# Optimization experiments

Measured on AMD Instinct MI355X. Metric: run time of the kernel, lower is better.

The kernel has to match this reference:

```python
import jax, jax.numpy as jnp
import numpy as np

N_HEAD = 4

def _conv1x1(x, W, b):
    # x: (N, C, W, H), W: (Cout, Cin), b: (Cout,) -- 1x1 conv == channel matmul
    return jnp.einsum('nchw,oc->nohw', x, W) + b[None, :, None, None]

def setup_inputs() -> dict:
    key = jax.random.key(0)
    ks = jax.random.split(key, 8)
    B, T, Tq, C, R = 16, 128, 64, 64, 16
    s = 0.05
    return {
        'qq': jax.random.normal(ks[0], (B * Tq, C, R, R), dtype=jnp.float32),
        'kv': jax.random.normal(ks[1], (B, T, C, R, R), dtype=jnp.float32),
        'Wq': jax.random.normal(ks[2], (C, C), dtype=jnp.float32) * s,
        'bq': jnp.zeros((C,), dtype=jnp.float32),
        'Wk': jax.random.normal(ks[3], (C, C), dtype=jnp.float32) * s,
        'bk': jnp.zeros((C,), dtype=jnp.float32),
        'Wv': jax.random.normal(ks[4], (C, C), dtype=jnp.float32) * s,
        'bv': jnp.zeros((C,), dtype=jnp.float32),
    }

def reference(qq, kv, Wq, bq, Wk, bk, Wv, bv):
    B, T, C, W, H = kv.shape
    dh = C // N_HEAD
    kvf = kv.reshape(-1, C, W, H)  # (B*T, C, W, H)
    # project and split heads: (B, n, S, dh, W, H)
    q = _conv1x1(qq, Wq, bq).reshape(B, -1, N_HEAD, dh, W, H).transpose(0, 2, 1, 3, 4, 5)
    k = _conv1x1(kvf, Wk, bk).reshape(B, -1, N_HEAD, dh, W, H).transpose(0, 2, 1, 3, 4, 5)
    v = _conv1x1(kvf, Wv, bv).reshape(B, -1, N_HEAD, dh, W, H).transpose(0, 2, 1, 3, 4, 5)
    scale = 1.0 / np.sqrt(W * H * dh).astype(np.float32)
    sim = jnp.einsum('bnkcwh,bntcwh->bnkt', q, k) * scale
    sim = jax.nn.softmax(sim, axis=-1)
    out = jnp.einsum('bnkt,bntcwh->bnkcwh', sim, v)
    out = out.transpose(0, 2, 1, 3, 4, 5).reshape(qq.shape)
    return out, sim
```

## Files before the change

kernel.cpp:

```cpp
#include <hip/hip_runtime.h>
#include <hip/hip_bf16.h>
#include <stdint.h>
#include <stddef.h>

#define DEVI __device__ __forceinline__

typedef __attribute__((ext_vector_type(8)))  short bf16x8;
typedef __attribute__((ext_vector_type(4)))  float f32x4;
typedef __attribute__((ext_vector_type(16))) float f32x16;
typedef __attribute__((ext_vector_type(2)))  unsigned u32x2;

DEVI unsigned short f2bf(float f) {
    __hip_bfloat16 h = __float2bfloat16(f);
    union { __hip_bfloat16 h; unsigned short u; } v; v.h = h; return v.u;
}
DEVI unsigned pk2(float lo, float hi) {
    return (unsigned)f2bf(lo) | ((unsigned)f2bf(hi) << 16);
}
DEVI f32x4 zero4() { f32x4 z; z[0] = z[1] = z[2] = z[3] = 0.f; return z; }
DEVI f32x16 zero16() {
    f32x16 z;
#pragma unroll
    for (int i = 0; i < 16; ++i) z[i] = 0.f;
    return z;
}


DEVI void load_wfrags(const float* __restrict__ W, const float* __restrict__ B,
                      int l15, int lg, bf16x8 (&bf)[4][2], float (&bias)[4]) {
#pragma unroll
    for (int ot = 0; ot < 4; ++ot) {
        const int o = ot * 16 + l15;
        bias[ot] = B[o];
#pragma unroll
        for (int ks = 0; ks < 2; ++ks) {
            const float* wp = W + o * 64 + ks * 32 + lg * 8;
            f32x4 w0 = *(const f32x4*)wp, w1 = *(const f32x4*)(wp + 4);
            bf16x8 a;
#pragma unroll
            for (int j = 0; j < 4; ++j) { a[j] = (short)f2bf(w0[j]); a[4 + j] = (short)f2bf(w1[j]); }
            bf[ot][ks] = a;
        }
    }
}

DEVI void proj_emit(unsigned short* __restrict__ S, const bf16x8 (&afr)[4][2],
                    const bf16x8 (&bf)[4][2], const float (&bias)[4],
                    int tid, int w, int l15, int lg,
                    unsigned short* __restrict__ og) {
#pragma unroll
    for (int pt = 0; pt < 4; ++pt) {
        const int p = w * 64 + pt * 16 + lg * 4;
#pragma unroll
        for (int ot = 0; ot < 4; ++ot) {
            const int o = ot * 16 + l15;
            f32x4 a1 = zero4();
            a1 = __builtin_amdgcn_mfma_f32_16x16x32_bf16(afr[pt][0], bf[ot][0], a1, 0, 0, 0);
            a1 = __builtin_amdgcn_mfma_f32_16x16x32_bf16(afr[pt][1], bf[ot][1], a1, 0, 0, 0);
            u32x2 sv;
            sv[0] = pk2(a1[0] + bias[ot], a1[1] + bias[ot]);
            sv[1] = pk2(a1[2] + bias[ot], a1[3] + bias[ot]);
            *(u32x2*)(&S[o * 264 + p]) = sv;
        }
    }
    __syncthreads();
#pragma unroll
    for (int it = 0; it < 8; ++it) {
        const int idx = it * 256 + tid;
        const int o = idx >> 5, px = (idx & 31) * 8;
        f32x4 vv = *(const f32x4*)(&S[o * 264 + px]);
        *(f32x4*)(og + (size_t)o * 256 + px) = vv;
    }
}

__global__ __launch_bounds__(256) void proj_q_kernel(
    const float* __restrict__ qq, const float* __restrict__ Wq,
    const float* __restrict__ bq, unsigned short* __restrict__ qbf)
{
    __shared__ unsigned short S[64 * 264];
    const int tid = threadIdx.x;
    const int w = tid >> 6, lane = tid & 63;
    const int l15 = lane & 15, lg = lane >> 4;
    const int n = blockIdx.x;
    const float* xg = qq + (size_t)n * 16384;

#pragma unroll
    for (int it = 0; it < 16; ++it) {
        const float* src = xg + it * 1024 + tid * 4;
        f32x4 xv = *(const f32x4*)src;
        u32x2 dd; dd[0] = pk2(xv[0], xv[1]); dd[1] = pk2(xv[2], xv[3]);
        *(u32x2*)(&S[(it * 4 + w) * 260 + lane * 4]) = dd;
    }
    bf16x8 bf1[4][2]; float bias1[4];
    load_wfrags(Wq, bq, l15, lg, bf1, bias1);
    __syncthreads();

    bf16x8 afr[4][2];
#pragma unroll
    for (int pt = 0; pt < 4; ++pt) {
        const int p0 = w * 64 + pt * 16;
#pragma unroll
        for (int ks = 0; ks < 2; ++ks) {
            bf16x8 e;
#pragma unroll
            for (int j = 0; j < 8; ++j)
                e[j] = (short)S[(ks * 32 + lg * 8 + j) * 260 + p0 + l15];
            afr[pt][ks] = e;
        }
    }
    __syncthreads();

    proj_emit(S, afr, bf1, bias1, tid, w, l15, lg, qbf + (size_t)n * 16384);
}

__global__ __launch_bounds__(256) void proj_kv_kernel(
    const float* __restrict__ kvg,
    const float* __restrict__ Wk, const float* __restrict__ bk,
    const float* __restrict__ Wv, const float* __restrict__ bv,
    unsigned short* __restrict__ kbf, unsigned short* __restrict__ vbf)
{
    __shared__ unsigned short S[64 * 264];
    const int tid = threadIdx.x;
    const int w = tid >> 6, lane = tid & 63;
    const int l15 = lane & 15, lg = lane >> 4;
    const int n = blockIdx.x;
    const float* xg = kvg + (size_t)n * 16384;

#pragma unroll
    for (int it = 0; it < 16; ++it) {
        const float* src = xg + it * 1024 + tid * 4;
        f32x4 xv = *(const f32x4*)src;
        u32x2 dd; dd[0] = pk2(xv[0], xv[1]); dd[1] = pk2(xv[2], xv[3]);
        *(u32x2*)(&S[(it * 4 + w) * 260 + lane * 4]) = dd;
    }
    bf16x8 bf1[4][2]; float bias1[4];
    load_wfrags(Wk, bk, l15, lg, bf1, bias1);
    __syncthreads();

    bf16x8 afr[4][2];
#pragma unroll
    for (int pt = 0; pt < 4; ++pt) {
        const int p0 = w * 64 + pt * 16;
#pragma unroll
        for (int ks = 0; ks < 2; ++ks) {
            bf16x8 e;
#pragma unroll
            for (int j = 0; j < 8; ++j)
                e[j] = (short)S[(ks * 32 + lg * 8 + j) * 260 + p0 + l15];
            afr[pt][ks] = e;
        }
    }
    __syncthreads();

    proj_emit(S, afr, bf1, bias1, tid, w, l15, lg, kbf + (size_t)n * 16384);
    __syncthreads();
    load_wfrags(Wv, bv, l15, lg, bf1, bias1);
    proj_emit(S, afr, bf1, bias1, tid, w, l15, lg, vbf + (size_t)n * 16384);
}

__global__ __launch_bounds__(128) void sim_kernel(
    const unsigned short* __restrict__ qbf, const unsigned short* __restrict__ kbf,
    float* __restrict__ partial)
{
    const int tid = threadIdx.x;
    const int w = tid >> 6, lane = tid & 63;
    const int l31 = lane & 31, lh = lane >> 5;
    const int bh = blockIdx.x & 63, ks = blockIdx.x >> 6;
    const int b = bh >> 2, head = bh & 3;
    const int t0 = w * 64;

    const unsigned short* qbase = qbf + (size_t)b * 64 * 16384 + head * 4096;
    const unsigned short* kbase = kbf + (size_t)b * 128 * 16384 + head * 4096;

    f32x16 acc00 = zero16(), acc01 = zero16(), acc10 = zero16(), acc11 = zero16();
    const int kk0 = ks * 1024;
    for (int kk = 0; kk < 64; ++kk) {
        int k = kk0 + kk * 16 + lh * 8;
        bf16x8 a0 = *(const bf16x8*)(qbase + (size_t)(l31)      * 16384 + k);
        bf16x8 a1 = *(const bf16x8*)(qbase + (size_t)(l31 + 32) * 16384 + k);
        bf16x8 b0 = *(const bf16x8*)(kbase + (size_t)(t0 + l31)      * 16384 + k);
        bf16x8 b1 = *(const bf16x8*)(kbase + (size_t)(t0 + 32 + l31) * 16384 + k);
        acc00 = __builtin_amdgcn_mfma_f32_32x32x16_bf16(a0, b0, acc00, 0, 0, 0);
        acc01 = __builtin_amdgcn_mfma_f32_32x32x16_bf16(a0, b1, acc01, 0, 0, 0);
        acc10 = __builtin_amdgcn_mfma_f32_32x32x16_bf16(a1, b0, acc10, 0, 0, 0);
        acc11 = __builtin_amdgcn_mfma_f32_32x32x16_bf16(a1, b1, acc11, 0, 0, 0);
    }

    float* pb = partial + ((size_t)ks * 4096 + (size_t)bh * 64) * 128;
#pragma unroll
    for (int r = 0; r < 16; ++r) {
        int kqr = (r & 3) + 8 * (r >> 2) + 4 * lh;
        pb[(kqr)      * 128 + t0 + l31]      = acc00[r];
        pb[(kqr)      * 128 + t0 + 32 + l31] = acc01[r];
        pb[(kqr + 32) * 128 + t0 + l31]      = acc10[r];
        pb[(kqr + 32) * 128 + t0 + 32 + l31] = acc11[r];
    }
}

__global__ __launch_bounds__(256) void softmax_kernel(
    const float* __restrict__ partial, float* __restrict__ sim_out,
    unsigned short* __restrict__ pbf)
{
    const int tid = threadIdx.x;
    const int w = tid >> 6, lane = tid & 63;
    const int row = blockIdx.x * 4 + w;

    float x0 = 0.f, x1 = 0.f;
#pragma unroll
    for (int s = 0; s < 4; ++s) {
        x0 += partial[((size_t)s * 4096 + row) * 128 + lane];
        x1 += partial[((size_t)s * 4096 + row) * 128 + 64 + lane];
    }
    const float scale = 1.0f / 64.0f;
    x0 *= scale; x1 *= scale;
    float m = fmaxf(x0, x1);
#pragma unroll
    for (int off = 32; off; off >>= 1) m = fmaxf(m, __shfl_xor(m, off));
    float e0 = __expf(x0 - m), e1 = __expf(x1 - m);
    float s = e0 + e1;
#pragma unroll
    for (int off = 32; off; off >>= 1) s += __shfl_xor(s, off);
    float inv = 1.0f / s;
    float p0 = e0 * inv, p1 = e1 * inv;
    sim_out[(size_t)row * 128 + lane]      = p0;
    sim_out[(size_t)row * 128 + 64 + lane] = p1;
    pbf[(size_t)row * 128 + lane]      = f2bf(p0);
    pbf[(size_t)row * 128 + 64 + lane] = f2bf(p1);
}

__global__ __launch_bounds__(256) void pv_kernel(
    const unsigned short* __restrict__ pbf, const unsigned short* __restrict__ vbf,
    float* __restrict__ outp)
{
    const int tid = threadIdx.x;
    const int w = tid >> 6, lane = tid & 63;
    const int l31 = lane & 31, lh = lane >> 5;
    const int bh = blockIdx.x >> 4, cb = blockIdx.x & 15;
    const int b = bh >> 2, h = bh & 3;
    const int ch = h * 16 + cb;
    const int p0 = w * 64;

    const unsigned short* pb = pbf + (size_t)bh * 64 * 128;
    const unsigned short* vb = vbf + (size_t)b * 128 * 16384 + (size_t)ch * 256;

    f32x16 acc00 = zero16(), acc01 = zero16(), acc10 = zero16(), acc11 = zero16();
    for (int kk = 0; kk < 8; ++kk) {
        const int t0 = kk * 16;
        bf16x8 a0 = *(const bf16x8*)(pb + (size_t)l31 * 128 + t0 + lh * 8);
        bf16x8 a1 = *(const bf16x8*)(pb + (size_t)(l31 + 32) * 128 + t0 + lh * 8);
        bf16x8 b0, b1;
#pragma unroll
        for (int j = 0; j < 8; ++j) {
            const unsigned short* vr = vb + (size_t)(t0 + lh * 8 + j) * 16384;
            b0[j] = (short)vr[p0 + l31];
            b1[j] = (short)vr[p0 + 32 + l31];
        }
        acc00 = __builtin_amdgcn_mfma_f32_32x32x16_bf16(a0, b0, acc00, 0, 0, 0);
        acc01 = __builtin_amdgcn_mfma_f32_32x32x16_bf16(a0, b1, acc01, 0, 0, 0);
        acc10 = __builtin_amdgcn_mfma_f32_32x32x16_bf16(a1, b0, acc10, 0, 0, 0);
        acc11 = __builtin_amdgcn_mfma_f32_32x32x16_bf16(a1, b1, acc11, 0, 0, 0);
    }

    float* ob = outp + (size_t)b * 64 * 16384 + (size_t)ch * 256;
#pragma unroll
    for (int r = 0; r < 16; ++r) {
        int kqr = (r & 3) + 8 * (r >> 2) + 4 * lh;
        ob[(size_t)(kqr)      * 16384 + p0 + l31]      = acc00[r];
        ob[(size_t)(kqr)      * 16384 + p0 + 32 + l31] = acc01[r];
        ob[(size_t)(kqr + 32) * 16384 + p0 + l31]      = acc10[r];
        ob[(size_t)(kqr + 32) * 16384 + p0 + 32 + l31] = acc11[r];
    }
}

extern "C" void kernel_launch(void* const* d_in, const int* in_sizes, int n_in,
                              void* d_out, int out_size, void* d_ws, size_t ws_size,
                              hipStream_t stream)
{
    const float* qq = (const float*)d_in[0];
    const float* kv = (const float*)d_in[1];
    const float* Wq = (const float*)d_in[2];
    const float* bq = (const float*)d_in[3];
    const float* Wk = (const float*)d_in[4];
    const float* bk = (const float*)d_in[5];
    const float* Wv = (const float*)d_in[6];
    const float* bv = (const float*)d_in[7];

    float* outp    = (float*)d_out;
    float* sim_out = outp + (size_t)16777216;

    char* ws = (char*)d_ws;
    unsigned short* qbf     = (unsigned short*)(ws);
    unsigned short* kbf     = (unsigned short*)(ws + 33554432);
    unsigned short* vbf     = (unsigned short*)(ws + 100663296);
    float*          partial = (float*)         (ws + 167772160);
    unsigned short* pbf     = (unsigned short*)(ws + 176160768);
    (void)in_sizes; (void)n_in; (void)out_size; (void)ws_size;

    proj_kv_kernel<<<dim3(2048), dim3(256), 0, stream>>>(kv, Wk, bk, Wv, bv, kbf, vbf);
    proj_q_kernel <<<dim3(1024), dim3(256), 0, stream>>>(qq, Wq, bq, qbf);
    sim_kernel    <<<dim3(256),  dim3(128), 0, stream>>>(qbf, kbf, partial);
    softmax_kernel<<<dim3(1024), dim3(256), 0, stream>>>(partial, sim_out, pbf);
    pv_kernel     <<<dim3(1024), dim3(256), 0, stream>>>(pbf, vbf, outp);
}
```

Baseline: 156.8 us.

## Retile sim kernel into more blocks and drop block barriers in projection epilogue

The sim kernel is re-split so that each block handles a 16-row query tile against 128 keys for one K-slice, using 16x16x32 MFMAs. This raises the grid from 256 to 1024 blocks to fill more CUs, and a block-index swizzle groups blocks that share K rows to help L2 reuse. The projection epilogue now has each wave read back only the LDS columns it wrote itself, which removes the __syncthreads between the MFMA stores and the global writes. The V weight fragments are also preloaded next to the K fragments. The cost is more global/L2 reads of K per query tile and higher register use from the second weight-fragment set.

```diff
diff --git a/kernel.cpp b/kernel.cpp
--- a/kernel.cpp
+++ b/kernel.cpp
@@ -26,6 +26,9 @@
 }
 
 
+#define XS 260
+#define OS 264
+
 DEVI void load_wfrags(const float* __restrict__ W, const float* __restrict__ B,
                       int l15, int lg, bf16x8 (&bf)[4][2], float (&bias)[4]) {
 #pragma unroll
@@ -46,7 +49,7 @@
 
 DEVI void proj_emit(unsigned short* __restrict__ S, const bf16x8 (&afr)[4][2],
                     const bf16x8 (&bf)[4][2], const float (&bias)[4],
-                    int tid, int w, int l15, int lg,
+                    int w, int lane, int l15, int lg,
                     unsigned short* __restrict__ og) {
 #pragma unroll
     for (int pt = 0; pt < 4; ++pt) {
@@ -60,15 +63,14 @@
             u32x2 sv;
             sv[0] = pk2(a1[0] + bias[ot], a1[1] + bias[ot]);
             sv[1] = pk2(a1[2] + bias[ot], a1[3] + bias[ot]);
-            *(u32x2*)(&S[o * 264 + p]) = sv;
-        }
-    }
-    __syncthreads();
+            *(u32x2*)(&S[o * OS + p]) = sv;
+        }
+    }
 #pragma unroll
     for (int it = 0; it < 8; ++it) {
-        const int idx = it * 256 + tid;
-        const int o = idx >> 5, px = (idx & 31) * 8;
-        f32x4 vv = *(const f32x4*)(&S[o * 264 + px]);
+        const int o  = it * 8 + (lane >> 3);
+        const int px = w * 64 + (lane & 7) * 8;
+        f32x4 vv = *(const f32x4*)(&S[o * OS + px]);
         *(f32x4*)(og + (size_t)o * 256 + px) = vv;
     }
 }
@@ -77,7 +79,7 @@
     const float* __restrict__ qq, const float* __restrict__ Wq,
     const float* __restrict__ bq, unsigned short* __restrict__ qbf)
 {
-    __shared__ unsigned short S[64 * 264];
+    __shared__ unsigned short S[64 * OS];
     const int tid = threadIdx.x;
     const int w = tid >> 6, lane = tid & 63;
     const int l15 = lane & 15, lg = lane >> 4;
@@ -89,7 +91,7 @@
         const float* src = xg + it * 1024 + tid * 4;
         f32x4 xv = *(const f32x4*)src;
         u32x2 dd; dd[0] = pk2(xv[0], xv[1]); dd[1] = pk2(xv[2], xv[3]);
-        *(u32x2*)(&S[(it * 4 + w) * 260 + lane * 4]) = dd;
+        *(u32x2*)(&S[(it * 4 + w) * XS + lane * 4]) = dd;
     }
     bf16x8 bf1[4][2]; float bias1[4];
     load_wfrags(Wq, bq, l15, lg, bf1, bias1);
@@ -104,13 +106,13 @@
             bf16x8 e;
 #pragma unroll
             for (int j = 0; j < 8; ++j)
-                e[j] = (short)S[(ks * 32 + lg * 8 + j) * 260 + p0 + l15];
+                e[j] = (short)S[(ks * 32 + lg * 8 + j) * XS + p0 + l15];
             afr[pt][ks] = e;
         }
     }
     __syncthreads();
 
-    proj_emit(S, afr, bf1, bias1, tid, w, l15, lg, qbf + (size_t)n * 16384);
+    proj_emit(S, afr, bf1, bias1, w, lane, l15, lg, qbf + (size_t)n * 16384);
 }
 
 __global__ __launch_bounds__(256) void proj_kv_kernel(
@@ -119,7 +121,7 @@
     const float* __restrict__ Wv, const float* __restrict__ bv,
     unsigned short* __restrict__ kbf, unsigned short* __restrict__ vbf)
 {
-    __shared__ unsigned short S[64 * 264];
+    __shared__ unsigned short S[64 * OS];
     const int tid = threadIdx.x;
     const int w = tid >> 6, lane = tid & 63;
     const int l15 = lane & 15, lg = lane >> 4;
@@ -131,10 +133,11 @@
         const float* src = xg + it * 1024 + tid * 4;
         f32x4 xv = *(const f32x4*)src;
         u32x2 dd; dd[0] = pk2(xv[0], xv[1]); dd[1] = pk2(xv[2], xv[3]);
-        *(u32x2*)(&S[(it * 4 + w) * 260 + lane * 4]) = dd;
-    }
-    bf16x8 bf1[4][2]; float bias1[4];
+        *(u32x2*)(&S[(it * 4 + w) * XS + lane * 4]) = dd;
+    }
+    bf16x8 bf1[4][2], bf2[4][2]; float bias1[4], bias2[4];
     load_wfrags(Wk, bk, l15, lg, bf1, bias1);
+    load_wfrags(Wv, bv, l15, lg, bf2, bias2);
     __syncthreads();
 
     bf16x8 afr[4][2];
@@ -146,16 +149,14 @@
             bf16x8 e;
 #pragma unroll
             for (int j = 0; j < 8; ++j)
-                e[j] = (short)S[(ks * 32 + lg * 8 + j) * 260 + p0 + l15];
+                e[j] = (short)S[(ks * 32 + lg * 8 + j) * XS + p0 + l15];
             afr[pt][ks] = e;
         }
     }
     __syncthreads();
 
-    proj_emit(S, afr, bf1, bias1, tid, w, l15, lg, kbf + (size_t)n * 16384);
-    __syncthreads();
-    load_wfrags(Wv, bv, l15, lg, bf1, bias1);
-    proj_emit(S, afr, bf1, bias1, tid, w, l15, lg, vbf + (size_t)n * 16384);
+    proj_emit(S, afr, bf1, bias1, w, lane, l15, lg, kbf + (size_t)n * 16384);
+    proj_emit(S, afr, bf2, bias2, w, lane, l15, lg, vbf + (size_t)n * 16384);
 }
 
 __global__ __launch_bounds__(128) void sim_kernel(
@@ -164,37 +165,36 @@
 {
     const int tid = threadIdx.x;
     const int w = tid >> 6, lane = tid & 63;
-    const int l31 = lane & 31, lh = lane >> 5;
-    const int bh = blockIdx.x & 63, ks = blockIdx.x >> 6;
-    const int b = bh >> 2, head = bh & 3;
-    const int t0 = w * 64;
-
-    const unsigned short* qbase = qbf + (size_t)b * 64 * 16384 + head * 4096;
-    const unsigned short* kbase = kbf + (size_t)b * 128 * 16384 + head * 4096;
-
-    f32x16 acc00 = zero16(), acc01 = zero16(), acc10 = zero16(), acc11 = zero16();
-    const int kk0 = ks * 1024;
-    for (int kk = 0; kk < 64; ++kk) {
-        int k = kk0 + kk * 16 + lh * 8;
-        bf16x8 a0 = *(const bf16x8*)(qbase + (size_t)(l31)      * 16384 + k);
-        bf16x8 a1 = *(const bf16x8*)(qbase + (size_t)(l31 + 32) * 16384 + k);
-        bf16x8 b0 = *(const bf16x8*)(kbase + (size_t)(t0 + l31)      * 16384 + k);
-        bf16x8 b1 = *(const bf16x8*)(kbase + (size_t)(t0 + 32 + l31) * 16384 + k);
-        acc00 = __builtin_amdgcn_mfma_f32_32x32x16_bf16(a0, b0, acc00, 0, 0, 0);
-        acc01 = __builtin_amdgcn_mfma_f32_32x32x16_bf16(a0, b1, acc01, 0, 0, 0);
-        acc10 = __builtin_amdgcn_mfma_f32_32x32x16_bf16(a1, b0, acc10, 0, 0, 0);
-        acc11 = __builtin_amdgcn_mfma_f32_32x32x16_bf16(a1, b1, acc11, 0, 0, 0);
-    }
-
-    float* pb = partial + ((size_t)ks * 4096 + (size_t)bh * 64) * 128;
-#pragma unroll
-    for (int r = 0; r < 16; ++r) {
-        int kqr = (r & 3) + 8 * (r >> 2) + 4 * lh;
-        pb[(kqr)      * 128 + t0 + l31]      = acc00[r];
-        pb[(kqr)      * 128 + t0 + 32 + l31] = acc01[r];
-        pb[(kqr + 32) * 128 + t0 + l31]      = acc10[r];
-        pb[(kqr + 32) * 128 + t0 + 32 + l31] = acc11[r];
-    }
+    const int l15 = lane & 15, lg = lane >> 4;
+    const int bid = blockIdx.x;
+    const int l = (bid & 7) * 128 + (bid >> 3);
+    const int kq4 = l & 3, ks = (l >> 2) & 3, bh = l >> 4;
+    const int b = bh >> 2, h = bh & 3;
+
+    const unsigned short* qp = qbf + ((size_t)b * 64 + kq4 * 16 + l15) * 16384
+                                   + h * 4096 + ks * 1024 + lg * 8;
+    const unsigned short* kp = kbf + ((size_t)b * 128 + w * 64 + l15) * 16384
+                                   + h * 4096 + ks * 1024 + lg * 8;
+
+    f32x4 acc[4];
+#pragma unroll
+    for (int tt = 0; tt < 4; ++tt) acc[tt] = zero4();
+
+    for (int kk = 0; kk < 32; ++kk) {
+        bf16x8 a = *(const bf16x8*)(qp + kk * 32);
+#pragma unroll
+        for (int tt = 0; tt < 4; ++tt) {
+            bf16x8 bfr = *(const bf16x8*)(kp + (size_t)tt * 16 * 16384 + kk * 32);
+            acc[tt] = __builtin_amdgcn_mfma_f32_16x16x32_bf16(a, bfr, acc[tt], 0, 0, 0);
+        }
+    }
+
+    float* pb = partial + ((size_t)ks * 4096 + (size_t)bh * 64 + kq4 * 16) * 128 + w * 64;
+#pragma unroll
+    for (int tt = 0; tt < 4; ++tt)
+#pragma unroll
+        for (int r = 0; r < 4; ++r)
+            pb[(lg * 4 + r) * 128 + tt * 16 + l15] = acc[tt][r];
 }
 
 __global__ __launch_bounds__(256) void softmax_kernel(
@@ -298,7 +298,7 @@
 
     proj_kv_kernel<<<dim3(2048), dim3(256), 0, stream>>>(kv, Wk, bk, Wv, bv, kbf, vbf);
     proj_q_kernel <<<dim3(1024), dim3(256), 0, stream>>>(qq, Wq, bq, qbf);
-    sim_kernel    <<<dim3(256),  dim3(128), 0, stream>>>(qbf, kbf, partial);
+    sim_kernel    <<<dim3(1024), dim3(128), 0, stream>>>(qbf, kbf, partial);
     softmax_kernel<<<dim3(1024), dim3(256), 0, stream>>>(partial, sim_out, pbf);
     pv_kernel     <<<dim3(1024), dim3(256), 0, stream>>>(pbf, vbf, outp);
 }
```

After: 177.2 us. +13.0%, slower.
